# Kernel optimization log

Measured on AMD Instinct MI355X. Metric: run time of the kernel, lower is better.

The kernel has to match this reference:

```python
import jax, jax.numpy as jnp
import numpy as np
from jax.ops import segment_sum

NEG_SLOPE = 0.2
N0, N1, N2, N3 = 100000, 300000, 150000, 50000
DIN, DMID = 64, 128


def setup_inputs() -> dict:
    key = jax.random.key(0)
    ks = jax.random.split(key, 16)
    g = lambda k, shp, fan_in: jax.random.normal(k, shp, dtype=jnp.float32) * (1.0 / np.sqrt(fan_in))
    return {
        "x_0": jax.random.normal(ks[0], (N0, DIN), dtype=jnp.float32),
        "x_1": jax.random.normal(ks[1], (N1, DIN), dtype=jnp.float32),
        "x_2": jax.random.normal(ks[2], (N2, DIN), dtype=jnp.float32),
        "x_3": jax.random.normal(ks[3], (N3, DIN), dtype=jnp.float32),
        "x_4": jax.random.normal(ks[4], (10000, DIN), dtype=jnp.float32),
        # COO indices: row 0 = destination (row of sparse matrix), row 1 = source (column)
        "adj0_idx": jax.random.randint(ks[5], (2, 800000), 0, N0),
        "adj3_idx": jax.random.randint(ks[6], (2, 800000), 0, N3),
        "inc01_t": jax.random.randint(ks[7], (600000,), 0, N0),   # rows of incidence_0_1 (0-cells)
        "inc01_s": jax.random.randint(ks[8], (600000,), 0, N1),   # cols (1-cells)
        "inc23_t": jax.random.randint(ks[9], (200000,), 0, N2),   # rows of incidence_2_3 (2-cells)
        "inc23_s": jax.random.randint(ks[10], (200000,), 0, N3),  # cols (3-cells)
        "W_hbs0": g(ks[11], (DIN, DMID), DIN),
        "W_hbs3": g(ks[12], (DIN, DMID), DIN),
        "W_s01": g(ks[13], (DIN, DMID), DIN),   # HBNS source weight: x_1 -> target-rank (0) messages
        "W_t23": g(ks[14], (DIN, DMID), DIN),   # HBNS target weight: x_2 -> source-rank (3) messages
        "fc0_W": g(ks[15], (DMID, DMID), DMID),
        "fc0_b": jnp.zeros((DMID,), dtype=jnp.float32),
        "fc3_W": g(jax.random.fold_in(key, 100), (DMID, DMID), DMID),
        "fc3_b": jnp.zeros((DMID,), dtype=jnp.float32),
    }


def _spmm(msg, dst, src, n_out):
    # out[i] = sum_{(i,j) in nnz} msg[j]  == sparse_matrix @ msg
    return segment_sum(msg[src], dst, num_segments=n_out)


def reference(x_0, x_1, x_2, x_3, x_4, adj0_idx, adj3_idx, inc01_t, inc01_s,
              inc23_t, inc23_s, W_hbs0, W_hbs3, W_s01, W_t23,
              fc0_W, fc0_b, fc3_W, fc3_b):
    lrelu = lambda v: jax.nn.leaky_relu(v, NEG_SLOPE)
    # HBS within-rank propagation: A @ (x W)
    x_0_to_0 = _spmm(x_0 @ W_hbs0, adj0_idx[0], adj0_idx[1], x_0.shape[0])
    x_3_to_3 = _spmm(x_3 @ W_hbs3, adj3_idx[0], adj3_idx[1], x_3.shape[0])
    # HBNS cross-rank propagation
    # message on target rank 0: incidence_0_1 @ (x_1 W_s)
    x_1_to_0 = _spmm(x_1 @ W_s01, inc01_t, inc01_s, x_0.shape[0])
    # message on source rank 3: incidence_2_3^T @ (x_2 W_t)
    x_2_to_3 = _spmm(x_2 @ W_t23, inc23_s, inc23_t, x_3.shape[0])
    # sum aggregation + FC + LeakyReLU
    x_0_new = lrelu((x_0_to_0 + x_1_to_0) @ fc0_W.T + fc0_b)
    x_3_new = lrelu((x_2_to_3 + x_3_to_3) @ fc3_W.T + fc3_b)
    return (x_0_new, x_1, x_2, x_3_new, x_4)
```

## Files before the change

### kernel.cpp

```cpp
#include <hip/hip_runtime.h>

#define NEG_SLOPE 0.2f
#define PSHIFT 15
#define MAXP 16
#define EPB 2048


__device__ __forceinline__ int decode_dst(int j, const int* ad0, const int* d1,
                                          const int* ad3, const int* d2,
                                          int E0, int E01, int E3,
                                          int n0, int n3) {
    if (j < E0) return ad0[j];
    if ((j -= E0) < E01) return n0 + d1[j];
    if ((j -= E01) < E3) return 2 * n0 + ad3[j];
    return 2 * n0 + n3 + d2[j - E3];
}

__device__ __forceinline__ int decode_src(int j, const int* as0, const int* s1,
                                          const int* as3, const int* s2,
                                          int E0, int E01, int E3) {
    if (j < E0) return as0[j];
    if ((j -= E0) < E01) return s1[j];
    if ((j -= E01) < E3) return as3[j];
    return s2[j - E3];
}

__global__ __launch_bounds__(256) void bin_sizes(const int* __restrict__ ad0,
                                                 const int* __restrict__ d1,
                                                 const int* __restrict__ ad3,
                                                 const int* __restrict__ d2,
                                                 int E0, int E01, int E3, int E23,
                                                 int n0, int n3,
                                                 int* __restrict__ gsizes) {
    __shared__ int h[MAXP];
    if (threadIdx.x < MAXP) h[threadIdx.x] = 0;
    __syncthreads();
    int T = E0 + E01 + E3 + E23;
    int stride = gridDim.x * 256;
    for (int i = blockIdx.x * 256 + threadIdx.x; i < T; i += stride) {
        int cd = decode_dst(i, ad0, d1, ad3, d2, E0, E01, E3, n0, n3);
        atomicAdd(&h[cd >> PSHIFT], 1);
    }
    __syncthreads();
    if (threadIdx.x < MAXP) atomicAdd(&gsizes[threadIdx.x], h[threadIdx.x]);
}

__global__ void scan16(const int* __restrict__ gsizes,
                       int* __restrict__ pstart, int* __restrict__ bcursor) {
    if (threadIdx.x == 0 && blockIdx.x == 0) {
        int run = 0;
        for (int p = 0; p < MAXP; ++p) {
            pstart[p] = run;
            bcursor[p] = run;
            run += gsizes[p];
        }
        pstart[MAXP] = run;
    }
}

__global__ __launch_bounds__(256) void bin_scatter(const int* __restrict__ ad0,
                                                   const int* __restrict__ as0,
                                                   const int* __restrict__ d1,
                                                   const int* __restrict__ s1,
                                                   const int* __restrict__ ad3,
                                                   const int* __restrict__ as3,
                                                   const int* __restrict__ d2,
                                                   const int* __restrict__ s2,
                                                   int E0, int E01, int E3, int E23,
                                                   int n0, int n3,
                                                   int* __restrict__ bcursor,
                                                   int2* __restrict__ bucket) {
    __shared__ int h[MAXP], base[MAXP], loc[MAXP];
    int t = threadIdx.x;
    if (t < MAXP) { h[t] = 0; loc[t] = 0; }
    __syncthreads();

    int T = E0 + E01 + E3 + E23;
    int b0 = blockIdx.x * EPB;
    int cd[EPB / 256], sv[EPB / 256];
    bool ok[EPB / 256];
#pragma unroll
    for (int j = 0; j < EPB / 256; ++j) {
        int idx = b0 + j * 256 + t;
        ok[j] = idx < T;
        if (ok[j]) {
            cd[j] = decode_dst(idx, ad0, d1, ad3, d2, E0, E01, E3, n0, n3);
            sv[j] = decode_src(idx, as0, s1, as3, s2, E0, E01, E3);
            atomicAdd(&h[cd[j] >> PSHIFT], 1);
        }
    }
    __syncthreads();
    if (t < MAXP && h[t] > 0) base[t] = atomicAdd(&bcursor[t], h[t]);
    __syncthreads();
#pragma unroll
    for (int j = 0; j < EPB / 256; ++j) {
        if (ok[j]) {
            int p = cd[j] >> PSHIFT;
            int o = atomicAdd(&loc[p], 1);
            bucket[base[p] + o] = make_int2(cd[j], sv[j]);
        }
    }
}

__global__ __launch_bounds__(256) void hist_part(const int2* __restrict__ bucket,
                                                 const int* __restrict__ pstart,
                                                 int* __restrict__ counts, int BPC) {
    int p = blockIdx.x & (MAXP - 1);
    int r = blockIdx.x >> 4;
    int beg = pstart[p], end = pstart[p + 1];
    int stride = BPC * 256;
    for (int i = beg + r * 256 + (int)threadIdx.x; i < end; i += stride)
        atomicAdd(&counts[bucket[i].x], 1);
}

__global__ __launch_bounds__(256) void chunk_sum(const int* __restrict__ counts,
                                                 int* __restrict__ bsum, int NT) {
    __shared__ int red[256];
    int base = blockIdx.x * 2048;
    int t = threadIdx.x;
    int s = 0;
#pragma unroll
    for (int j = 0; j < 8; ++j) {
        int idx = base + j * 256 + t;
        if (idx < NT) s += counts[idx];
    }
    red[t] = s;
    __syncthreads();
    for (int off = 128; off > 0; off >>= 1) {
        if (t < off) red[t] += red[t + off];
        __syncthreads();
    }
    if (t == 0) bsum[blockIdx.x] = red[0];
}

__global__ __launch_bounds__(256) void scan_bsum(const int* __restrict__ bsum,
                                                 int* __restrict__ bbase, int nb) {
    __shared__ int sh[256];
    int t = threadIdx.x;
    int v = (t < nb) ? bsum[t] : 0;
    sh[t] = v;
    __syncthreads();
    for (int off = 1; off < 256; off <<= 1) {
        int add = (t >= off) ? sh[t - off] : 0;
        __syncthreads();
        sh[t] += add;
        __syncthreads();
    }
    if (t < nb) bbase[t] = sh[t] - v;
}

__global__ __launch_bounds__(256) void chunk_scan(const int* __restrict__ counts,
                                                  const int* __restrict__ bbase,
                                                  int* __restrict__ offsets,
                                                  int* __restrict__ cursors,
                                                  int NT, int E_total) {
    __shared__ int tsum[256];
    int t = threadIdx.x;
    int base = blockIdx.x * 2048 + t * 8;
    int v[8];
    int s = 0;
#pragma unroll
    for (int j = 0; j < 8; ++j) {
        int idx = base + j;
        v[j] = (idx < NT) ? counts[idx] : 0;
        s += v[j];
    }
    tsum[t] = s;
    __syncthreads();
    for (int off = 1; off < 256; off <<= 1) {
        int add = (t >= off) ? tsum[t - off] : 0;
        __syncthreads();
        tsum[t] += add;
        __syncthreads();
    }
    int run = bbase[blockIdx.x] + tsum[t] - s;
#pragma unroll
    for (int j = 0; j < 8; ++j) {
        int idx = base + j;
        if (idx < NT) { offsets[idx] = run; cursors[idx] = run; }
        run += v[j];
    }
    if (blockIdx.x == 0 && t == 0) offsets[NT] = E_total;
}

__global__ __launch_bounds__(256) void part_fill(const int2* __restrict__ bucket,
                                                 const int* __restrict__ pstart,
                                                 int* __restrict__ cursors,
                                                 int* __restrict__ edge_src, int BPC) {
    int p = blockIdx.x & (MAXP - 1);
    int r = blockIdx.x >> 4;
    int beg = pstart[p], end = pstart[p + 1];
    int stride = BPC * 256;
    for (int i = beg + r * 256 + (int)threadIdx.x; i < end; i += stride) {
        int2 e = bucket[i];
        int pos = atomicAdd(&cursors[e.x], 1);
        edge_src[pos] = e.y;
    }
}

__global__ __launch_bounds__(256) void gather4(const int* __restrict__ offsets,
                                               const int* __restrict__ edge_src,
                                               const float* __restrict__ x0,
                                               const float* __restrict__ x1,
                                               const float* __restrict__ x2,
                                               const float* __restrict__ x3,
                                               float* __restrict__ agg0,
                                               float* __restrict__ agg3,
                                               int n0, int n3) {
    const int NT = 2 * n0 + 2 * n3;
    int row = blockIdx.x * 16 + (threadIdx.x >> 4);
    int c4 = (threadIdx.x & 15) * 4;
    if (row >= NT) return;
    const float* xs;
    float* outp;
    if (row < n0)               { xs = x0; outp = &agg0[(size_t)row * 128]; }
    else if (row < 2 * n0)      { xs = x1; outp = &agg0[(size_t)(row - n0) * 128 + 64]; }
    else if (row < 2 * n0 + n3) { xs = x3; outp = &agg3[(size_t)(row - 2 * n0) * 128]; }
    else                        { xs = x2; outp = &agg3[(size_t)(row - 2 * n0 - n3) * 128 + 64]; }

    int k = offsets[row], end = offsets[row + 1];
    float4 acc = make_float4(0.f, 0.f, 0.f, 0.f);
    for (; k + 2 <= end; k += 2) {
        int i0 = edge_src[k];
        int i1 = edge_src[k + 1];
        float4 a = *(const float4*)&xs[(size_t)i0 * 64 + c4];
        float4 b = *(const float4*)&xs[(size_t)i1 * 64 + c4];
        acc.x += a.x + b.x;
        acc.y += a.y + b.y;
        acc.z += a.z + b.z;
        acc.w += a.w + b.w;
    }
    if (k < end) {
        int i0 = edge_src[k];
        float4 a = *(const float4*)&xs[(size_t)i0 * 64 + c4];
        acc.x += a.x; acc.y += a.y; acc.z += a.z; acc.w += a.w;
    }
    *(float4*)&outp[c4] = acc;
}

__global__ __launch_bounds__(256) void combine_w2(const float* __restrict__ Wtop0,
                                                  const float* __restrict__ Wbot0,
                                                  const float* __restrict__ F0,
                                                  float* __restrict__ WC0,
                                                  const float* __restrict__ Wtop3,
                                                  const float* __restrict__ Wbot3,
                                                  const float* __restrict__ F3,
                                                  float* __restrict__ WC3) {
    int gi = blockIdx.x * 256 + threadIdx.x;
    int which = gi >> 14;
    int i = gi & 16383;
    const float* Wtop = which ? Wtop3 : Wtop0;
    const float* Wbot = which ? Wbot3 : Wbot0;
    const float* F = which ? F3 : F0;
    float* WC = which ? WC3 : WC0;
    int k = i >> 7;
    int c = i & 127;
    const float* wrow = (k < 64) ? &Wtop[(size_t)k * 128] : &Wbot[(size_t)(k - 64) * 128];
    const float* frow = &F[(size_t)c * 128];
    float s = 0.f;
#pragma unroll 8
    for (int j = 0; j < 128; j += 4) {
        float4 w = *(const float4*)&wrow[j];
        float4 f = *(const float4*)&frow[j];
        s = fmaf(w.x, f.x, s);
        s = fmaf(w.y, f.y, s);
        s = fmaf(w.z, f.z, s);
        s = fmaf(w.w, f.w, s);
    }
    WC[(size_t)k * 128 + c] = s;
}

__global__ __launch_bounds__(256) void fc_lrelu(const float* __restrict__ A,
                                                const float* __restrict__ WC,
                                                const float* __restrict__ bias,
                                                float* __restrict__ Y, int n) {
    __shared__ float WS[64][128];
    __shared__ float XS[64][68];
    const int t = threadIdx.x;
    const int row0 = blockIdx.x * 64;
    const int c = (t & 31) * 4;
    const int rbase = (t >> 5) * 8;
    float acc[8][4];
#pragma unroll
    for (int i = 0; i < 8; ++i)
#pragma unroll
        for (int j = 0; j < 4; ++j) acc[i][j] = 0.f;

    for (int p = 0; p < 2; ++p) {
        __syncthreads();
        const float4* Wp4 = (const float4*)(WC + (size_t)p * 64 * 128);
        float4* WS4 = (float4*)&WS[0][0];
        for (int i = t; i < 2048; i += 256) WS4[i] = Wp4[i];
        for (int i = t; i < 64 * 16; i += 256) {
            int r = i >> 4, c4 = i & 15;
            float4 v = make_float4(0.f, 0.f, 0.f, 0.f);
            if (row0 + r < n)
                v = *(const float4*)&A[(size_t)(row0 + r) * 128 + p * 64 + c4 * 4];
            *(float4*)&XS[r][c4 * 4] = v;
        }
        __syncthreads();

#pragma unroll 4
        for (int k = 0; k < 64; k += 4) {
            float4 w[4];
            w[0] = *(const float4*)&WS[k + 0][c];
            w[1] = *(const float4*)&WS[k + 1][c];
            w[2] = *(const float4*)&WS[k + 2][c];
            w[3] = *(const float4*)&WS[k + 3][c];
#pragma unroll
            for (int i = 0; i < 8; ++i) {
                float4 x = *(const float4*)&XS[rbase + i][k];
                float xs[4] = {x.x, x.y, x.z, x.w};
#pragma unroll
                for (int kk = 0; kk < 4; ++kk) {
                    acc[i][0] = fmaf(xs[kk], w[kk].x, acc[i][0]);
                    acc[i][1] = fmaf(xs[kk], w[kk].y, acc[i][1]);
                    acc[i][2] = fmaf(xs[kk], w[kk].z, acc[i][2]);
                    acc[i][3] = fmaf(xs[kk], w[kk].w, acc[i][3]);
                }
            }
        }
    }

    float4 b = *(const float4*)&bias[c];
    float bs[4] = {b.x, b.y, b.z, b.w};
#pragma unroll
    for (int i = 0; i < 8; ++i) {
        int r = row0 + rbase + i;
        if (r < n) {
            float o[4];
#pragma unroll
            for (int j = 0; j < 4; ++j) {
                float v = acc[i][j] + bs[j];
                o[j] = v > 0.f ? v : NEG_SLOPE * v;
            }
            *(float4*)&Y[(size_t)r * 128 + c] = make_float4(o[0], o[1], o[2], o[3]);
        }
    }
}

__global__ __launch_bounds__(256) void copy_all(const float4* __restrict__ s1, float4* __restrict__ o1, int m1,
                                                const float4* __restrict__ s2, float4* __restrict__ o2, int m2,
                                                const float4* __restrict__ s4, float4* __restrict__ o4, int m4) {
    int total = m1 + m2 + m4;
    int i = blockIdx.x * 256 + threadIdx.x;
    int stride = gridDim.x * 256;
    for (; i < total; i += stride) {
        int j = i;
        if (j < m1) { o1[j] = s1[j]; }
        else if ((j -= m1) < m2) { o2[j] = s2[j]; }
        else { j -= m2; o4[j] = s4[j]; }
    }
}

extern "C" void kernel_launch(void* const* d_in, const int* in_sizes, int n_in,
                              void* d_out, int out_size, void* d_ws, size_t ws_size,
                              hipStream_t stream) {
    const float* x0 = (const float*)d_in[0];
    const float* x1 = (const float*)d_in[1];
    const float* x2 = (const float*)d_in[2];
    const float* x3 = (const float*)d_in[3];
    const float* x4 = (const float*)d_in[4];
    const int* adj0 = (const int*)d_in[5];
    const int* adj3 = (const int*)d_in[6];
    const int* inc01_t = (const int*)d_in[7];
    const int* inc01_s = (const int*)d_in[8];
    const int* inc23_t = (const int*)d_in[9];
    const int* inc23_s = (const int*)d_in[10];
    const float* W_hbs0 = (const float*)d_in[11];
    const float* W_hbs3 = (const float*)d_in[12];
    const float* W_s01 = (const float*)d_in[13];
    const float* W_t23 = (const float*)d_in[14];
    const float* fc0_W = (const float*)d_in[15];
    const float* fc0_b = (const float*)d_in[16];
    const float* fc3_W = (const float*)d_in[17];
    const float* fc3_b = (const float*)d_in[18];

    const int n0 = in_sizes[0] / 64, n1 = in_sizes[1] / 64;
    const int n2 = in_sizes[2] / 64, n3 = in_sizes[3] / 64, n4 = in_sizes[4] / 64;
    const int E0 = in_sizes[5] / 2, E3 = in_sizes[6] / 2;
    const int E01 = in_sizes[7], E23 = in_sizes[9];
    const int NT = 2 * n0 + 2 * n3;
    const int E_total = E0 + E01 + E3 + E23;
    const int nb = (NT + 2047) / 2048;
    const int BPC = 64;

    float* ws = (float*)d_ws;
    size_t off = 0;
    float* agg0 = ws + off; off += (size_t)n0 * 128;
    float* agg3 = ws + off; off += (size_t)n3 * 128;
    float* wc0 = ws + off;  off += 16384;
    float* wc3 = ws + off;  off += 16384;
    int* counts = (int*)(ws + off);   off += NT;
    int* gsizes = (int*)(ws + off);   off += MAXP;
    int* offsets = (int*)(ws + off);  off += NT + 1;
    int* cursors = (int*)(ws + off);  off += NT;
    int* bsum = (int*)(ws + off);     off += 256;
    int* bbase = (int*)(ws + off);    off += 256;
    int* pstart = (int*)(ws + off);   off += MAXP + 1;
    int* bcursor = (int*)(ws + off);  off += MAXP;
    off = (off + 1) & ~(size_t)1;
    int2* bucket = (int2*)(ws + off); off += (size_t)E_total * 2;
    int* edge_src = (int*)(ws + off); off += E_total;

    float* out = (float*)d_out;
    float* o_x0 = out;
    float* o_x1 = o_x0 + (size_t)n0 * 128;
    float* o_x2 = o_x1 + (size_t)n1 * 64;
    float* o_x3 = o_x2 + (size_t)n2 * 64;
    float* o_x4 = o_x3 + (size_t)n3 * 128;

    hipMemsetAsync(counts, 0, (size_t)(NT + MAXP) * sizeof(int), stream);
    bin_sizes<<<2048, 256, 0, stream>>>(adj0, inc01_t, adj3, inc23_s,
                                        E0, E01, E3, E23, n0, n3, gsizes);
    scan16<<<1, 64, 0, stream>>>(gsizes, pstart, bcursor);
    bin_scatter<<<(E_total + EPB - 1) / EPB, 256, 0, stream>>>(
        adj0, adj0 + E0, inc01_t, inc01_s, adj3, adj3 + E3, inc23_s, inc23_t,
        E0, E01, E3, E23, n0, n3, bcursor, bucket);
    hist_part<<<MAXP * BPC, 256, 0, stream>>>(bucket, pstart, counts, BPC);
    chunk_sum<<<nb, 256, 0, stream>>>(counts, bsum, NT);
    scan_bsum<<<1, 256, 0, stream>>>(bsum, bbase, nb);
    chunk_scan<<<nb, 256, 0, stream>>>(counts, bbase, offsets, cursors, NT, E_total);
    part_fill<<<MAXP * BPC, 256, 0, stream>>>(bucket, pstart, cursors, edge_src, BPC);

    gather4<<<(NT + 15) / 16, 256, 0, stream>>>(offsets, edge_src, x0, x1, x2, x3,
                                                agg0, agg3, n0, n3);

    combine_w2<<<128, 256, 0, stream>>>(W_hbs0, W_s01, fc0_W, wc0,
                                        W_hbs3, W_t23, fc3_W, wc3);
    fc_lrelu<<<(n0 + 63) / 64, 256, 0, stream>>>(agg0, wc0, fc0_b, o_x0, n0);
    fc_lrelu<<<(n3 + 63) / 64, 256, 0, stream>>>(agg3, wc3, fc3_b, o_x3, n3);

    copy_all<<<8192, 256, 0, stream>>>((const float4*)x1, (float4*)o_x1, n1 * 16,
                                       (const float4*)x2, (float4*)o_x2, n2 * 16,
                                       (const float4*)x4, (float4*)o_x4, n4 * 16);
}
```

Measured before the change: 809.1 us.

## Replace per-row CSR build with two-level bucketing and LDS-accumulated gather

Replaces the full per-destination-row counting sort (histogram, three-stage scan, atomic fill) with a coarse partition followed by a refinement into 128-row fine buckets. The gather then processes one fine bucket per block, accumulating rows in shared memory with LDS atomics before writing the aggregates out. This drops several kernel launches and the per-row global atomics and scans. In exchange it reads and writes a second edge bucket array, does scalar 64-lane loads instead of float4, and makes float summation order nondeterministic.

```diff
diff --git a/kernel.cpp b/kernel.cpp
--- a/kernel.cpp
+++ b/kernel.cpp
@@ -1,9 +1,13 @@
 #include <hip/hip_runtime.h>
 
 #define NEG_SLOPE 0.2f
-#define PSHIFT 15
+#define FSHIFT 7
+#define FROWS 128
+#define MAXFINE 4096
+#define CSHIFT 15
 #define MAXP 16
-#define EPB 2048
+#define EPB1 2048
+#define EPB2 4096
 
 
 __device__ __forceinline__ int decode_dst(int j, const int* ad0, const int* d1,
@@ -25,37 +29,61 @@
     return s2[j - E3];
 }
 
-__global__ __launch_bounds__(256) void bin_sizes(const int* __restrict__ ad0,
+__global__ __launch_bounds__(256) void fine_hist(const int* __restrict__ ad0,
                                                  const int* __restrict__ d1,
                                                  const int* __restrict__ ad3,
                                                  const int* __restrict__ d2,
                                                  int E0, int E01, int E3, int E23,
-                                                 int n0, int n3,
-                                                 int* __restrict__ gsizes) {
-    __shared__ int h[MAXP];
-    if (threadIdx.x < MAXP) h[threadIdx.x] = 0;
+                                                 int n0, int n3, int NFINE,
+                                                 int* __restrict__ fsizes) {
+    __shared__ int h[MAXFINE];
+    int t = threadIdx.x;
+    for (int f = t; f < NFINE; f += 256) h[f] = 0;
     __syncthreads();
     int T = E0 + E01 + E3 + E23;
     int stride = gridDim.x * 256;
-    for (int i = blockIdx.x * 256 + threadIdx.x; i < T; i += stride) {
+    for (int i = blockIdx.x * 256 + t; i < T; i += stride) {
         int cd = decode_dst(i, ad0, d1, ad3, d2, E0, E01, E3, n0, n3);
-        atomicAdd(&h[cd >> PSHIFT], 1);
-    }
-    __syncthreads();
-    if (threadIdx.x < MAXP) atomicAdd(&gsizes[threadIdx.x], h[threadIdx.x]);
-}
-
-__global__ void scan16(const int* __restrict__ gsizes,
-                       int* __restrict__ pstart, int* __restrict__ bcursor) {
-    if (threadIdx.x == 0 && blockIdx.x == 0) {
-        int run = 0;
-        for (int p = 0; p < MAXP; ++p) {
-            pstart[p] = run;
-            bcursor[p] = run;
-            run += gsizes[p];
-        }
-        pstart[MAXP] = run;
-    }
+        atomicAdd(&h[cd >> FSHIFT], 1);
+    }
+    __syncthreads();
+    for (int f = t; f < NFINE; f += 256)
+        if (h[f]) atomicAdd(&fsizes[f], h[f]);
+}
+
+__global__ __launch_bounds__(256) void scan_fine(const int* __restrict__ fsizes,
+                                                 int NFINE, int NP, int E_total,
+                                                 int* __restrict__ fstart,
+                                                 int* __restrict__ fcursor4,
+                                                 int* __restrict__ bcursor) {
+    __shared__ int tsum[256];
+    int t = threadIdx.x;
+    int v[16];
+    int s = 0;
+#pragma unroll
+    for (int j = 0; j < 16; ++j) {
+        int f = t * 16 + j;
+        v[j] = (f < NFINE) ? fsizes[f] : 0;
+        s += v[j];
+    }
+    tsum[t] = s;
+    __syncthreads();
+    for (int off = 1; off < 256; off <<= 1) {
+        int a = (t >= off) ? tsum[t - off] : 0;
+        __syncthreads();
+        tsum[t] += a;
+        __syncthreads();
+    }
+    int run = tsum[t] - s;
+#pragma unroll
+    for (int j = 0; j < 16; ++j) {
+        int f = t * 16 + j;
+        if (f < NFINE) { fstart[f] = run; fcursor4[f * 4] = run; }
+        run += v[j];
+    }
+    if (t == 0) fstart[NFINE] = E_total;
+    __syncthreads();
+    if (t < NP) bcursor[t] = fstart[t * 256];
 }
 
 __global__ __launch_bounds__(256) void bin_scatter(const int* __restrict__ ad0,
@@ -69,173 +97,127 @@
                                                    int E0, int E01, int E3, int E23,
                                                    int n0, int n3,
                                                    int* __restrict__ bcursor,
-                                                   int2* __restrict__ bucket) {
+                                                   int2* __restrict__ bucket1) {
     __shared__ int h[MAXP], base[MAXP], loc[MAXP];
     int t = threadIdx.x;
     if (t < MAXP) { h[t] = 0; loc[t] = 0; }
     __syncthreads();
 
     int T = E0 + E01 + E3 + E23;
-    int b0 = blockIdx.x * EPB;
-    int cd[EPB / 256], sv[EPB / 256];
-    bool ok[EPB / 256];
-#pragma unroll
-    for (int j = 0; j < EPB / 256; ++j) {
+    int b0 = blockIdx.x * EPB1;
+    int cd[EPB1 / 256], sv[EPB1 / 256];
+    bool ok[EPB1 / 256];
+#pragma unroll
+    for (int j = 0; j < EPB1 / 256; ++j) {
         int idx = b0 + j * 256 + t;
         ok[j] = idx < T;
         if (ok[j]) {
             cd[j] = decode_dst(idx, ad0, d1, ad3, d2, E0, E01, E3, n0, n3);
             sv[j] = decode_src(idx, as0, s1, as3, s2, E0, E01, E3);
-            atomicAdd(&h[cd[j] >> PSHIFT], 1);
+            atomicAdd(&h[cd[j] >> CSHIFT], 1);
         }
     }
     __syncthreads();
     if (t < MAXP && h[t] > 0) base[t] = atomicAdd(&bcursor[t], h[t]);
     __syncthreads();
 #pragma unroll
-    for (int j = 0; j < EPB / 256; ++j) {
+    for (int j = 0; j < EPB1 / 256; ++j) {
         if (ok[j]) {
-            int p = cd[j] >> PSHIFT;
+            int p = cd[j] >> CSHIFT;
             int o = atomicAdd(&loc[p], 1);
-            bucket[base[p] + o] = make_int2(cd[j], sv[j]);
+            bucket1[base[p] + o] = make_int2(cd[j], sv[j]);
         }
     }
 }
 
-__global__ __launch_bounds__(256) void hist_part(const int2* __restrict__ bucket,
-                                                 const int* __restrict__ pstart,
-                                                 int* __restrict__ counts, int BPC) {
-    int p = blockIdx.x & (MAXP - 1);
-    int r = blockIdx.x >> 4;
-    int beg = pstart[p], end = pstart[p + 1];
-    int stride = BPC * 256;
-    for (int i = beg + r * 256 + (int)threadIdx.x; i < end; i += stride)
-        atomicAdd(&counts[bucket[i].x], 1);
-}
-
-__global__ __launch_bounds__(256) void chunk_sum(const int* __restrict__ counts,
-                                                 int* __restrict__ bsum, int NT) {
-    __shared__ int red[256];
-    int base = blockIdx.x * 2048;
+__global__ __launch_bounds__(256) void refine(const int2* __restrict__ bucket1,
+                                              const int* __restrict__ fstart,
+                                              int* __restrict__ fcursor4,
+                                              int2* __restrict__ bucket2,
+                                              int E_total, int NFINE, int NP) {
+    __shared__ int h[512];
     int t = threadIdx.x;
-    int s = 0;
-#pragma unroll
-    for (int j = 0; j < 8; ++j) {
-        int idx = base + j * 256 + t;
-        if (idx < NT) s += counts[idx];
-    }
-    red[t] = s;
-    __syncthreads();
-    for (int off = 128; off > 0; off >>= 1) {
-        if (t < off) red[t] += red[t + off];
-        __syncthreads();
-    }
-    if (t == 0) bsum[blockIdx.x] = red[0];
-}
-
-__global__ __launch_bounds__(256) void scan_bsum(const int* __restrict__ bsum,
-                                                 int* __restrict__ bbase, int nb) {
-    __shared__ int sh[256];
+    h[t] = 0;
+    h[t + 256] = 0;
+    int c0 = blockIdx.x * EPB2;
+    int c1 = min(c0 + EPB2, E_total);
+    int p0 = 0;
+    for (int p = 1; p < NP; ++p)
+        if (fstart[p * 256] <= c0) p0 = p;
+    int wbase = p0 * 256;
+    __syncthreads();
+    for (int i = c0 + t; i < c1; i += 256) {
+        int w = (bucket1[i].x >> FSHIFT) - wbase;
+        if (w >= 0 && w < 512) atomicAdd(&h[w], 1);
+    }
+    __syncthreads();
+    for (int w = t; w < 512; w += 256) {
+        int c = h[w];
+        if (c > 0 && wbase + w < NFINE)
+            h[w] = atomicAdd(&fcursor4[(wbase + w) * 4], c);
+    }
+    __syncthreads();
+    for (int i = c0 + t; i < c1; i += 256) {
+        int2 e = bucket1[i];
+        int f = e.x >> FSHIFT;
+        int w = f - wbase;
+        int pos;
+        if (w >= 0 && w < 512) pos = atomicAdd(&h[w], 1);
+        else pos = atomicAdd(&fcursor4[f * 4], 1);
+        bucket2[pos] = e;
+    }
+}
+
+__global__ __launch_bounds__(256) void gather_lds(const int2* __restrict__ bucket2,
+                                                  const int* __restrict__ fstart,
+                                                  const float* __restrict__ x0,
+                                                  const float* __restrict__ x1,
+                                                  const float* __restrict__ x2,
+                                                  const float* __restrict__ x3,
+                                                  float* __restrict__ agg0,
+                                                  float* __restrict__ agg3,
+                                                  int n0, int n3, int NT) {
+    __shared__ float acc[FROWS * 64];
     int t = threadIdx.x;
-    int v = (t < nb) ? bsum[t] : 0;
-    sh[t] = v;
-    __syncthreads();
-    for (int off = 1; off < 256; off <<= 1) {
-        int add = (t >= off) ? sh[t - off] : 0;
-        __syncthreads();
-        sh[t] += add;
-        __syncthreads();
-    }
-    if (t < nb) bbase[t] = sh[t] - v;
-}
-
-__global__ __launch_bounds__(256) void chunk_scan(const int* __restrict__ counts,
-                                                  const int* __restrict__ bbase,
-                                                  int* __restrict__ offsets,
-                                                  int* __restrict__ cursors,
-                                                  int NT, int E_total) {
-    __shared__ int tsum[256];
-    int t = threadIdx.x;
-    int base = blockIdx.x * 2048 + t * 8;
-    int v[8];
-    int s = 0;
-#pragma unroll
-    for (int j = 0; j < 8; ++j) {
-        int idx = base + j;
-        v[j] = (idx < NT) ? counts[idx] : 0;
-        s += v[j];
-    }
-    tsum[t] = s;
-    __syncthreads();
-    for (int off = 1; off < 256; off <<= 1) {
-        int add = (t >= off) ? tsum[t - off] : 0;
-        __syncthreads();
-        tsum[t] += add;
-        __syncthreads();
-    }
-    int run = bbase[blockIdx.x] + tsum[t] - s;
-#pragma unroll
-    for (int j = 0; j < 8; ++j) {
-        int idx = base + j;
-        if (idx < NT) { offsets[idx] = run; cursors[idx] = run; }
-        run += v[j];
-    }
-    if (blockIdx.x == 0 && t == 0) offsets[NT] = E_total;
-}
-
-__global__ __launch_bounds__(256) void part_fill(const int2* __restrict__ bucket,
-                                                 const int* __restrict__ pstart,
-                                                 int* __restrict__ cursors,
-                                                 int* __restrict__ edge_src, int BPC) {
-    int p = blockIdx.x & (MAXP - 1);
-    int r = blockIdx.x >> 4;
-    int beg = pstart[p], end = pstart[p + 1];
-    int stride = BPC * 256;
-    for (int i = beg + r * 256 + (int)threadIdx.x; i < end; i += stride) {
-        int2 e = bucket[i];
-        int pos = atomicAdd(&cursors[e.x], 1);
-        edge_src[pos] = e.y;
-    }
-}
-
-__global__ __launch_bounds__(256) void gather4(const int* __restrict__ offsets,
-                                               const int* __restrict__ edge_src,
-                                               const float* __restrict__ x0,
-                                               const float* __restrict__ x1,
-                                               const float* __restrict__ x2,
-                                               const float* __restrict__ x3,
-                                               float* __restrict__ agg0,
-                                               float* __restrict__ agg3,
-                                               int n0, int n3) {
-    const int NT = 2 * n0 + 2 * n3;
-    int row = blockIdx.x * 16 + (threadIdx.x >> 4);
-    int c4 = (threadIdx.x & 15) * 4;
-    if (row >= NT) return;
-    const float* xs;
-    float* outp;
-    if (row < n0)               { xs = x0; outp = &agg0[(size_t)row * 128]; }
-    else if (row < 2 * n0)      { xs = x1; outp = &agg0[(size_t)(row - n0) * 128 + 64]; }
-    else if (row < 2 * n0 + n3) { xs = x3; outp = &agg3[(size_t)(row - 2 * n0) * 128]; }
-    else                        { xs = x2; outp = &agg3[(size_t)(row - 2 * n0 - n3) * 128 + 64]; }
-
-    int k = offsets[row], end = offsets[row + 1];
-    float4 acc = make_float4(0.f, 0.f, 0.f, 0.f);
-    for (; k + 2 <= end; k += 2) {
-        int i0 = edge_src[k];
-        int i1 = edge_src[k + 1];
-        float4 a = *(const float4*)&xs[(size_t)i0 * 64 + c4];
-        float4 b = *(const float4*)&xs[(size_t)i1 * 64 + c4];
-        acc.x += a.x + b.x;
-        acc.y += a.y + b.y;
-        acc.z += a.z + b.z;
-        acc.w += a.w + b.w;
-    }
-    if (k < end) {
-        int i0 = edge_src[k];
-        float4 a = *(const float4*)&xs[(size_t)i0 * 64 + c4];
-        acc.x += a.x; acc.y += a.y; acc.z += a.z; acc.w += a.w;
-    }
-    *(float4*)&outp[c4] = acc;
+    for (int i = t; i < FROWS * 64; i += 256) acc[i] = 0.f;
+    __syncthreads();
+
+    int f = blockIdx.x;
+    int beg = fstart[f], end = fstart[f + 1];
+    int w = t >> 6, lane = t & 63;
+    for (int i0 = beg + w * 4; i0 < end; i0 += 16) {
+        int cnt = min(4, end - i0);
+        int2 e[4];
+        float v[4];
+#pragma unroll
+        for (int k = 0; k < 4; ++k)
+            if (k < cnt) e[k] = bucket2[i0 + k];
+#pragma unroll
+        for (int k = 0; k < 4; ++k)
+            if (k < cnt) {
+                int cd = e[k].x, src = e[k].y;
+                const float* xs = (cd < n0) ? x0
+                                : (cd < 2 * n0) ? x1
+                                : (cd < 2 * n0 + n3) ? x3 : x2;
+                v[k] = xs[(size_t)src * 64 + lane];
+            }
+#pragma unroll
+        for (int k = 0; k < 4; ++k)
+            if (k < cnt) atomicAdd(&acc[(e[k].x & (FROWS - 1)) * 64 + lane], v[k]);
+    }
+    __syncthreads();
+
+    int g = t >> 4, l = t & 15;
+    for (int r = g; r < FROWS; r += 16) {
+        int cd = f * FROWS + r;
+        if (cd >= NT) break;
+        float* dst;
+        if (cd < n0)                dst = agg0 + (size_t)cd * 128;
+        else if (cd < 2 * n0)       dst = agg0 + (size_t)(cd - n0) * 128 + 64;
+        else if (cd < 2 * n0 + n3)  dst = agg3 + (size_t)(cd - 2 * n0) * 128;
+        else                        dst = agg3 + (size_t)(cd - 2 * n0 - n3) * 128 + 64;
+        *(float4*)&dst[l * 4] = *(float4*)&acc[r * 64 + l * 4];
+    }
 }
 
 __global__ __launch_bounds__(256) void combine_w2(const float* __restrict__ Wtop0,
@@ -261,11 +243,11 @@
 #pragma unroll 8
     for (int j = 0; j < 128; j += 4) {
         float4 w = *(const float4*)&wrow[j];
-        float4 f = *(const float4*)&frow[j];
-        s = fmaf(w.x, f.x, s);
-        s = fmaf(w.y, f.y, s);
-        s = fmaf(w.z, f.z, s);
-        s = fmaf(w.w, f.w, s);
+        float4 fv = *(const float4*)&frow[j];
+        s = fmaf(w.x, fv.x, s);
+        s = fmaf(w.y, fv.y, s);
+        s = fmaf(w.z, fv.z, s);
+        s = fmaf(w.w, fv.w, s);
     }
     WC[(size_t)k * 128 + c] = s;
 }
@@ -382,8 +364,8 @@
     const int E01 = in_sizes[7], E23 = in_sizes[9];
     const int NT = 2 * n0 + 2 * n3;
     const int E_total = E0 + E01 + E3 + E23;
-    const int nb = (NT + 2047) / 2048;
-    const int BPC = 64;
+    const int NFINE = (NT + FROWS - 1) >> FSHIFT;
+    const int NP = (NT + (1 << CSHIFT) - 1) >> CSHIFT;
 
     float* ws = (float*)d_ws;
     size_t off = 0;
@@ -391,17 +373,13 @@
     float* agg3 = ws + off; off += (size_t)n3 * 128;
     float* wc0 = ws + off;  off += 16384;
     float* wc3 = ws + off;  off += 16384;
-    int* counts = (int*)(ws + off);   off += NT;
-    int* gsizes = (int*)(ws + off);   off += MAXP;
-    int* offsets = (int*)(ws + off);  off += NT + 1;
-    int* cursors = (int*)(ws + off);  off += NT;
-    int* bsum = (int*)(ws + off);     off += 256;
-    int* bbase = (int*)(ws + off);    off += 256;
-    int* pstart = (int*)(ws + off);   off += MAXP + 1;
+    int* fsizes = (int*)(ws + off);   off += MAXFINE;
+    int* fstart = (int*)(ws + off);   off += MAXFINE + 1;
+    int* fcursor4 = (int*)(ws + off); off += (size_t)MAXFINE * 4;
     int* bcursor = (int*)(ws + off);  off += MAXP;
     off = (off + 1) & ~(size_t)1;
-    int2* bucket = (int2*)(ws + off); off += (size_t)E_total * 2;
-    int* edge_src = (int*)(ws + off); off += E_total;
+    int2* bucket1 = (int2*)(ws + off); off += (size_t)E_total * 2;
+    int2* bucket2 = (int2*)(ws + off); off += (size_t)E_total * 2;
 
     float* out = (float*)d_out;
     float* o_x0 = out;
@@ -410,21 +388,19 @@
     float* o_x3 = o_x2 + (size_t)n2 * 64;
     float* o_x4 = o_x3 + (size_t)n3 * 128;
 
-    hipMemsetAsync(counts, 0, (size_t)(NT + MAXP) * sizeof(int), stream);
-    bin_sizes<<<2048, 256, 0, stream>>>(adj0, inc01_t, adj3, inc23_s,
-                                        E0, E01, E3, E23, n0, n3, gsizes);
-    scan16<<<1, 64, 0, stream>>>(gsizes, pstart, bcursor);
-    bin_scatter<<<(E_total + EPB - 1) / EPB, 256, 0, stream>>>(
+    hipMemsetAsync(fsizes, 0, (size_t)MAXFINE * sizeof(int), stream);
+    fine_hist<<<128, 256, 0, stream>>>(adj0, inc01_t, adj3, inc23_s,
+                                       E0, E01, E3, E23, n0, n3, NFINE, fsizes);
+    scan_fine<<<1, 256, 0, stream>>>(fsizes, NFINE, NP, E_total,
+                                     fstart, fcursor4, bcursor);
+    bin_scatter<<<(E_total + EPB1 - 1) / EPB1, 256, 0, stream>>>(
         adj0, adj0 + E0, inc01_t, inc01_s, adj3, adj3 + E3, inc23_s, inc23_t,
-        E0, E01, E3, E23, n0, n3, bcursor, bucket);
-    hist_part<<<MAXP * BPC, 256, 0, stream>>>(bucket, pstart, counts, BPC);
-    chunk_sum<<<nb, 256, 0, stream>>>(counts, bsum, NT);
-    scan_bsum<<<1, 256, 0, stream>>>(bsum, bbase, nb);
-    chunk_scan<<<nb, 256, 0, stream>>>(counts, bbase, offsets, cursors, NT, E_total);
-    part_fill<<<MAXP * BPC, 256, 0, stream>>>(bucket, pstart, cursors, edge_src, BPC);
-
-    gather4<<<(NT + 15) / 16, 256, 0, stream>>>(offsets, edge_src, x0, x1, x2, x3,
-                                                agg0, agg3, n0, n3);
+        E0, E01, E3, E23, n0, n3, bcursor, bucket1);
+    refine<<<(E_total + EPB2 - 1) / EPB2, 256, 0, stream>>>(
+        bucket1, fstart, fcursor4, bucket2, E_total, NFINE, NP);
+
+    gather_lds<<<NFINE, 256, 0, stream>>>(bucket2, fstart, x0, x1, x2, x3,
+                                          agg0, agg3, n0, n3, NT);
 
     combine_w2<<<128, 256, 0, stream>>>(W_hbs0, W_s01, fc0_W, wc0,
                                         W_hbs3, W_t23, fc3_W, wc3);
```

Result: slower. 1.347 ms (+66.5%).
